# Kernel optimization log

Measured on AMD Instinct MI355X. Metric: run time of the kernel, lower is better.

The kernel has to match this reference:

```python
import jax, jax.numpy as jnp
import numpy as np

N, M, F_IN, F_OUT, B = 8192, 4096, 256, 128, 2048
NEG = -9e15
EPS = 1e-5


def leaky(x, slope=0.2):
    return jnp.where(x > 0, x, slope * x)


def batchnorm(x, gamma, beta):
    # BatchNorm1d training-mode semantics: biased batch stats over dim 0
    m = x.mean(axis=0)
    v = jnp.var(x, axis=0)
    return (x - m) * jax.lax.rsqrt(v + EPS) * gamma + beta


def setup_inputs() -> dict:
    key = jax.random.key(0)
    ks = jax.random.split(key, 12)
    inp = {}
    inp["Sinput"] = jax.random.normal(ks[0], (N, F_IN), dtype=jnp.float32)
    inp["Rinput"] = jax.random.normal(ks[1], (M, F_IN), dtype=jnp.float32)
    inp["inter_adj"] = jax.random.randint(ks[2], (N, M), 0, 2).astype(jnp.int32)
    inp["city_adj"] = jax.random.randint(ks[3], (N, N), 0, 2).astype(jnp.int32)
    inp["province_adj"] = jax.random.randint(ks[4], (N, N), 0, 2).astype(jnp.int32)
    inp["source_index"] = jax.random.randint(ks[5], (B,), 0, N).astype(jnp.int32)
    s_w = 1.414 * np.sqrt(6.0 / (F_IN + F_OUT))  # xavier_uniform gain=1.414
    s_a = 1.414 * np.sqrt(6.0 / (2 * F_OUT + 1))
    inp["W1"] = jax.random.uniform(ks[6], (F_IN, F_OUT), jnp.float32, -s_w, s_w)
    inp["W2"] = jax.random.uniform(ks[7], (F_IN, F_OUT), jnp.float32, -s_w, s_w)
    inp["a"] = jax.random.uniform(ks[8], (2 * F_OUT, 1), jnp.float32, -s_a, s_a)
    inp["a3"] = jax.random.uniform(ks[9], (2 * F_OUT, 1), jnp.float32, -s_a, s_a)
    inp["a4"] = jax.random.uniform(ks[10], (2 * F_OUT, 1), jnp.float32, -s_a, s_a)
    inp["bn1_gamma"] = jnp.ones((F_OUT,), jnp.float32)
    inp["bn1_beta"] = jnp.zeros((F_OUT,), jnp.float32)
    inp["bn2_gamma"] = jnp.ones((F_OUT,), jnp.float32)
    inp["bn2_beta"] = jnp.zeros((F_OUT,), jnp.float32)
    return inp


def reference(Sinput, Rinput, inter_adj, city_adj, province_adj, source_index,
              W1, W2, a, a3, a4, bn1_gamma, bn1_beta, bn2_gamma, bn2_beta):
    F = W1.shape[1]
    h1 = Rinput @ W1            # [M, F]
    h2 = Sinput @ W2            # [N, F]
    # Decomposed GAT score: cat([h1[m], h2[n]]) @ a == h1[m]@a[:F] + h2[n]@a[F:]
    e12 = leaky((h2 @ a[F:, 0])[:, None] + (h1 @ a[:F, 0])[None, :])  # [N, M]
    att_inter = jax.nn.softmax(jnp.where(inter_adj > 0, e12, NEG), axis=1)
    h2_ = h2[source_index]      # [B, F]
    # cat([h2_, h2_]) @ a3 -> h2_ @ (a3[:F] + a3[F:]), constant along N axis
    s3 = leaky(h2_ @ (a3[:F, 0] + a3[F:, 0]))  # [B]
    s4 = leaky(h2_ @ (a4[:F, 0] + a4[F:, 0]))  # [B]
    Nn = Sinput.shape[0]
    e3 = jnp.broadcast_to(s3[:, None], (s3.shape[0], Nn))
    e4 = jnp.broadcast_to(s4[:, None], (s4.shape[0], Nn))
    att3 = jax.nn.softmax(jnp.where(city_adj[source_index] > 0, e3, NEG), axis=1)
    att4 = jax.nn.softmax(jnp.where(province_adj[source_index] > 0, e4, NEG), axis=1)
    InterRC = att_inter @ h1                    # [N, F]
    IntraNC = att3.T @ h2_ + att4.T @ h2_       # [N, F]
    v_output = leaky(batchnorm(att_inter.T @ h2, bn1_gamma, bn1_beta))  # [M, F]
    u_output = leaky(batchnorm(InterRC + IntraNC, bn2_gamma, bn2_beta))  # [N, F]
    h_prime = u_output @ v_output.T             # [N, M]
    return jax.nn.elu(h_prime)
```

## Files before the change

### kernel.cpp

```cpp
#include <hip/hip_runtime.h>
#include <stdint.h>

#define N_ 8192
#define M_ 4096
#define FIN_ 256
#define F_ 128
#define B_ 2048

typedef __attribute__((ext_vector_type(8))) short vs8;
typedef __attribute__((ext_vector_type(8))) __bf16 vb8;
typedef __attribute__((ext_vector_type(4))) float vf4;

union ABu { vs8 s; vb8 b; };

__device__ __forceinline__ vf4 mfma16(const ABu& a, const ABu& b, vf4 c) {
    return __builtin_amdgcn_mfma_f32_16x16x32_bf16(a.b, b.b, c, 0, 0, 0);
}
__device__ __forceinline__ unsigned short f2b(float x) {
    union { float f; unsigned u; } v; v.f = x;
    unsigned r = v.u + 0x7fffu + ((v.u >> 16) & 1u);
    return (unsigned short)(r >> 16);
}
__device__ __forceinline__ float lrelu(float x) { return x > 0.f ? x : 0.2f * x; }

__device__ __forceinline__ void glds16(const unsigned short* g, void* l) {
    __builtin_amdgcn_global_load_lds((const __attribute__((address_space(1))) unsigned int*)g,
                                     (__attribute__((address_space(3))) unsigned int*)l, 16, 0, 0);
}

__global__ void k_prep(const float* __restrict__ W1, const float* __restrict__ W2,
                       unsigned short* __restrict__ W1T, unsigned short* __restrict__ W2T,
                       float4* __restrict__ Z, int nz4) {
    int id = blockIdx.x * 256 + threadIdx.x;
    if (id < 65536) {
        const float* W = (id < 32768) ? W1 : W2;
        unsigned short* WT = (id < 32768) ? W1T : W2T;
        int o = id & 32767;
        int f = o >> 8, k = o & 255;
        WT[o] = f2b(W[k * F_ + f]);
    } else {
        int z = id - 65536;
        if (z < nz4) Z[z] = make_float4(0.f, 0.f, 0.f, 0.f);
    }
}

__global__ __launch_bounds__(256) void k_hgemmF(const float* __restrict__ Rin, const float* __restrict__ Sin,
                                                const unsigned short* __restrict__ W1T,
                                                const unsigned short* __restrict__ W2T,
                                                const float* __restrict__ a,
                                                float* __restrict__ h2,
                                                unsigned short* __restrict__ h1P, unsigned short* __restrict__ h2P,
                                                float* __restrict__ s1, float* __restrict__ s2) {
    __shared__ unsigned short tb[16][136];
    __shared__ float sred[4][16];
    int t = threadIdx.x;
    int w = t >> 6, l = t & 63, lr = l & 15, lg = l >> 4;
    int gr = blockIdx.x * 16;
    const float* X; const unsigned short* WT; unsigned short* HP; float* sout; const float* av;
    int row0; bool isH2;
    if (gr < M_) { X = Rin; WT = W1T; HP = h1P; sout = s1; av = a;      row0 = gr;      isH2 = false; }
    else         { X = Sin; WT = W2T; HP = h2P; sout = s2; av = a + F_; row0 = gr - M_; isH2 = true;  }
    int fbase = w * 32;
    vf4 acc[2] = {};
    const float* xp = X + (size_t)(row0 + lr) * FIN_ + lg * 8;
#pragma unroll
    for (int kk = 0; kk < FIN_; kk += 32) {
        float4 xa = *(const float4*)(xp + kk);
        float4 xb = *(const float4*)(xp + kk + 4);
        ABu af;
        af.s[0] = (short)f2b(xa.x); af.s[1] = (short)f2b(xa.y);
        af.s[2] = (short)f2b(xa.z); af.s[3] = (short)f2b(xa.w);
        af.s[4] = (short)f2b(xb.x); af.s[5] = (short)f2b(xb.y);
        af.s[6] = (short)f2b(xb.z); af.s[7] = (short)f2b(xb.w);
#pragma unroll
        for (int q = 0; q < 2; ++q) {
            ABu bf; bf.s = *(const vs8*)(WT + (fbase + q * 16 + lr) * FIN_ + kk + lg * 8);
            acc[q] = mfma16(af, bf, acc[q]);
        }
    }
    if (isH2) {
#pragma unroll
        for (int q = 0; q < 2; ++q)
#pragma unroll
            for (int r = 0; r < 4; ++r)
                h2[(size_t)(row0 + lg * 4 + r) * F_ + fbase + q * 16 + lr] = acc[q][r];
    }
#pragma unroll
    for (int q = 0; q < 2; ++q)
#pragma unroll
        for (int r = 0; r < 4; ++r)
            tb[lg * 4 + r][fbase + q * 16 + lr] = f2b(acc[q][r]);
    float a0 = av[fbase + lr], a1 = av[fbase + 16 + lr];
    float tv[4];
#pragma unroll
    for (int r = 0; r < 4; ++r) tv[r] = acc[0][r] * a0 + acc[1][r] * a1;
#pragma unroll
    for (int off = 1; off < 16; off <<= 1)
#pragma unroll
        for (int r = 0; r < 4; ++r) tv[r] += __shfl_xor(tv[r], off, 64);
    if ((l & 15) == 0)
#pragma unroll
        for (int r = 0; r < 4; ++r) sred[w][lg * 4 + r] = tv[r];
    __syncthreads();
    {
        int f = t >> 1, half = t & 1;
        vs8 o;
#pragma unroll
        for (int j = 0; j < 8; ++j) o[j] = (short)tb[half * 8 + j][f];
        *(vs8*)(HP + ((size_t)(row0 >> 5) * 128 + f) * 32 + (row0 & 16) + half * 8) = o;
    }
    if (t < 16) {
        float s = sred[0][t] + sred[1][t] + sred[2][t] + sred[3][t];
        sout[row0 + t] = s;
    }
}

__global__ __launch_bounds__(256) void k_adjgather(const int* __restrict__ inter, const float* __restrict__ s1,
                                                   const float* __restrict__ s2, unsigned short* __restrict__ bm,
                                                   float* __restrict__ rowmax, float* __restrict__ rowinv,
                                                   const int* __restrict__ city, const int* __restrict__ prov,
                                                   const int* __restrict__ src,
                                                   uint32_t* __restrict__ BMtc, uint32_t* __restrict__ BMtp,
                                                   float* __restrict__ w3, float* __restrict__ w4,
                                                   const float* __restrict__ h2, unsigned short* __restrict__ h2wP) {
    __shared__ float wred[8];
    int t = threadIdx.x;
    int wv = t >> 6, ln = t & 63;
    if (blockIdx.x < N_) {
        int n = blockIdx.x;
        const int* rp = inter + (size_t)n * M_ + t * 16;
        float sv[16]; unsigned mask = 0;
#pragma unroll
        for (int c = 0; c < 4; ++c) {
            int4 v = *(const int4*)(rp + c * 4);
            if (v.x > 0) mask |= 1u << (c * 4 + 0);
            if (v.y > 0) mask |= 1u << (c * 4 + 1);
            if (v.z > 0) mask |= 1u << (c * 4 + 2);
            if (v.w > 0) mask |= 1u << (c * 4 + 3);
            float4 s = *(const float4*)(s1 + t * 16 + c * 4);
            sv[c * 4 + 0] = s.x; sv[c * 4 + 1] = s.y; sv[c * 4 + 2] = s.z; sv[c * 4 + 3] = s.w;
        }
        bm[(size_t)n * 256 + t] = (unsigned short)(mask & 0xffffu);
        float mx = -3.0e38f;
#pragma unroll
        for (int j = 0; j < 16; ++j) if (mask & (1u << j)) mx = fmaxf(mx, sv[j]);
        for (int off = 32; off > 0; off >>= 1) mx = fmaxf(mx, __shfl_down(mx, off, 64));
        if (ln == 0) wred[wv] = mx;
        __syncthreads();
        float s1mx = fmaxf(fmaxf(wred[0], wred[1]), fmaxf(wred[2], wred[3]));
        float s2n = s2[n];
        float rmx = lrelu(s2n + s1mx);
        float sum = 0.f;
#pragma unroll
        for (int j = 0; j < 16; ++j) if (mask & (1u << j)) sum += __expf(lrelu(s2n + sv[j]) - rmx);
        for (int off = 32; off > 0; off >>= 1) sum += __shfl_down(sum, off, 64);
        if (ln == 0) wred[4 + wv] = sum;
        __syncthreads();
        if (t == 0) {
            float tot = wred[4] + wred[5] + wred[6] + wred[7];
            bool any = s1mx > -2.9e38f;
            rowmax[n] = any ? rmx : 0.f;
            rowinv[n] = (any && tot > 0.f) ? 1.0f / tot : 0.f;
        }
    } else if (blockIdx.x < N_ + 2 * B_) {
        int bb = blockIdx.x - N_;
        int b = bb & (B_ - 1);
        bool isC = bb < B_;
        const int* adj = isC ? city : prov;
        uint32_t* BM = isC ? BMtc : BMtp;
        float* wout = isC ? w3 : w4;
        const int* rowp = adj + (size_t)src[b] * N_;
        int cnt = 0;
#pragma unroll 4
        for (int i = 0; i < N_ / 256; ++i) {
            int v = rowp[i * 256 + t];
            unsigned long long bal = __ballot(v > 0);
            cnt += (v > 0);
            if (ln == 0) {
                int widx = i * 8 + wv * 2;
                BM[(size_t)widx * B_ + b] = (uint32_t)bal;
                BM[(size_t)(widx + 1) * B_ + b] = (uint32_t)(bal >> 32);
            }
        }
        float fc = (float)cnt;
        for (int off = 32; off > 0; off >>= 1) fc += __shfl_down(fc, off, 64);
        if (ln == 0) wred[wv] = fc;
        __syncthreads();
        if (t == 0) {
            float tot = wred[0] + wred[1] + wred[2] + wred[3];
            wout[b] = tot > 0.f ? 1.0f / tot : 0.f;
        }
    } else {
        int bblk = blockIdx.x - (N_ + 2 * B_);
        int f = t & 127, halfb = t >> 7;
        vs8 o0, o1;
#pragma unroll
        for (int i = 0; i < 8; ++i) {
            int b0 = bblk * 32 + halfb * 16 + i;
            o0[i] = (short)f2b(h2[(size_t)src[b0] * F_ + f]);
            int b1 = b0 + 8;
            o1[i] = (short)f2b(h2[(size_t)src[b1] * F_ + f]);
        }
        unsigned short* dst = h2wP + ((size_t)bblk * 128 + f) * 32 + halfb * 16;
        *(vs8*)dst = o0;
        *(vs8*)(dst + 8) = o1;
    }
}

__global__ __launch_bounds__(256) void k_attmat2(const unsigned char* __restrict__ bm8,
                                                 const float* __restrict__ s1, const float* __restrict__ s2,
                                                 const float* __restrict__ rowmax, const float* __restrict__ rowinv,
                                                 unsigned short* __restrict__ attP,
                                                 unsigned short* __restrict__ attT) {
    __shared__ unsigned short tile[64][33];
    int bx = blockIdx.x;
    int mt = bx & 63, nt = bx >> 6;
    int nb = nt * 32, mb = mt * 64;
    int t = threadIdx.x;
    int mo = t & 7, nl = t >> 3;
    int n = nb + nl;
    int m = mb + mo * 8;
    unsigned bits = bm8[(size_t)n * 512 + (m >> 3)];
    float s2n = s2[n], rmx = rowmax[n], rin = rowinv[n];
    float4 sa = *(const float4*)(s1 + m);
    float4 sb = *(const float4*)(s1 + m + 4);
    float sv[8] = {sa.x, sa.y, sa.z, sa.w, sb.x, sb.y, sb.z, sb.w};
    vs8 o;
#pragma unroll
    for (int j = 0; j < 8; ++j) {
        float v = (bits & (1u << j)) ? __expf(lrelu(s2n + sv[j]) - rmx) * rin : 0.f;
        o[j] = (short)f2b(v);
        tile[mo * 8 + j][nl] = (unsigned short)o[j];
    }
    *(vs8*)(attP + ((size_t)(m >> 5) * N_ + n) * 32 + (m & 31)) = o;
    __syncthreads();
    int mr = t >> 2, sg = t & 3;
    vs8 ot;
#pragma unroll
    for (int j = 0; j < 8; ++j) ot[j] = (short)tile[mr][sg * 8 + j];
    *(vs8*)(attT + ((size_t)nt * M_ + mb + mr) * 32 + sg * 8) = ot;
}

__global__ __launch_bounds__(256) void k_gemmABC(const unsigned short* __restrict__ attP,
                                                 const unsigned short* __restrict__ attT,
                                                 const unsigned short* __restrict__ h1P,
                                                 const unsigned short* __restrict__ h2P,
                                                 const uint32_t* __restrict__ BMtc, const uint32_t* __restrict__ BMtp,
                                                 const float* __restrict__ w3, const float* __restrict__ w4,
                                                 const unsigned short* __restrict__ h2wP,
                                                 float* __restrict__ uP, float* __restrict__ vP) {
    __shared__ __align__(16) unsigned short smem[16384];
    int t = threadIdx.x;
    int w = t >> 6, l = t & 63;
    int lr = l & 15, lg = l >> 4;
    int bx = blockIdx.x;
    if (bx < 768) {
        bool isA = bx < 512;
        int i = isA ? bx : bx - 512;
        int x, y, ns, kbase, rowsK;
        const unsigned short* Asrc; const unsigned short* Bsrc; float* Out;
        if (isA) { x = i & 63; y = i >> 6; ns = 16; kbase = y * 16; rowsK = N_;
                   Asrc = attP; Bsrc = h1P; Out = uP + (size_t)y * N_ * F_; }
        else     { x = i & 31; y = i >> 5; ns = 32; kbase = y * 32; rowsK = M_;
                   Asrc = attT; Bsrc = h2P; Out = vP + (size_t)y * M_ * F_; }
        int rb0 = x * 128;
        int rq = (w >> 1) * 64;
        int cb = (w & 1) * 64;
        auto stage = [&](int kb, int buf) {
#pragma unroll
            for (int ii = 0; ii < 4; ++ii) {
                int c = w * 4 + ii;
                const unsigned short* g; int loff;
                if (c < 8) { g = Asrc + ((size_t)kb * rowsK + rb0) * 32 + c * 512 + l * 8;
                             loff = buf * 8192 + c * 512; }
                else       { g = Bsrc + (size_t)kb * 4096 + (c - 8) * 512 + l * 8;
                             loff = buf * 8192 + 4096 + (c - 8) * 512; }
                glds16(g, smem + loff);
            }
        };
        vf4 acc[4][4] = {};
        stage(kbase, 0);
        __syncthreads();
        int cur = 0;
        for (int step = 0; step < ns; ++step) {
            if (step + 1 < ns) stage(kbase + step + 1, cur ^ 1);
            const unsigned short* base = smem + cur * 8192;
            ABu a[4], b[4];
#pragma unroll
            for (int s = 0; s < 4; ++s) a[s].s = *(const vs8*)(base + (rq + s * 16 + lr) * 32 + lg * 8);
#pragma unroll
            for (int q = 0; q < 4; ++q) b[q].s = *(const vs8*)(base + 4096 + (cb + q * 16 + lr) * 32 + lg * 8);
#pragma unroll
            for (int s = 0; s < 4; ++s)
#pragma unroll
                for (int q = 0; q < 4; ++q) acc[s][q] = mfma16(a[s], b[q], acc[s][q]);
            __syncthreads();
            cur ^= 1;
        }
#pragma unroll
        for (int s = 0; s < 4; ++s)
#pragma unroll
            for (int q = 0; q < 4; ++q)
#pragma unroll
                for (int r = 0; r < 4; ++r)
                    Out[(size_t)(rb0 + rq + s * 16 + lg * 4 + r) * F_ + cb + q * 16 + lr] = acc[s][q][r];
    } else {
        int i = bx - 768;
        int xc = i & 127, yc = i >> 7;
        int nb0 = xc * 64 + (w & 1) * 32;
        int fb = (w >> 1) * 64;
        int wi = nb0 >> 5;
        const uint32_t* bc = BMtc + (size_t)wi * B_;
        const uint32_t* bp = BMtp + (size_t)wi * B_;
        vf4 acc[2][4] = {};
        int b0s = yc * (B_ / 4);
        for (int b0 = b0s; b0 < b0s + B_ / 4; b0 += 32) {
            int bb = b0 + lg * 8;
            uint4 c0 = *(const uint4*)(bc + bb);
            uint4 c1 = *(const uint4*)(bc + bb + 4);
            uint4 p0 = *(const uint4*)(bp + bb);
            uint4 p1 = *(const uint4*)(bp + bb + 4);
            float4 wa = *(const float4*)(w3 + bb);
            float4 wb = *(const float4*)(w3 + bb + 4);
            float4 wc = *(const float4*)(w4 + bb);
            float4 wd = *(const float4*)(w4 + bb + 4);
            const unsigned short* hb = h2wP + (size_t)(b0 >> 5) * 128 * 32;
            ABu bf0, bf1, bf2, bf3;
            bf0.s = *(const vs8*)(hb + (size_t)(fb + lr) * 32 + lg * 8);
            bf1.s = *(const vs8*)(hb + (size_t)(fb + 16 + lr) * 32 + lg * 8);
            bf2.s = *(const vs8*)(hb + (size_t)(fb + 32 + lr) * 32 + lg * 8);
            bf3.s = *(const vs8*)(hb + (size_t)(fb + 48 + lr) * 32 + lg * 8);
            uint32_t cw[8] = {c0.x, c0.y, c0.z, c0.w, c1.x, c1.y, c1.z, c1.w};
            uint32_t pw[8] = {p0.x, p0.y, p0.z, p0.w, p1.x, p1.y, p1.z, p1.w};
            float w3v[8] = {wa.x, wa.y, wa.z, wa.w, wb.x, wb.y, wb.z, wb.w};
            float w4v[8] = {wc.x, wc.y, wc.z, wc.w, wd.x, wd.y, wd.z, wd.w};
            ABu af0, af1;
#pragma unroll
            for (int j = 0; j < 8; ++j) {
                float v0 = (((cw[j] >> lr) & 1u) ? w3v[j] : 0.f) + (((pw[j] >> lr) & 1u) ? w4v[j] : 0.f);
                float v1 = (((cw[j] >> (16 + lr)) & 1u) ? w3v[j] : 0.f) + (((pw[j] >> (16 + lr)) & 1u) ? w4v[j] : 0.f);
                af0.s[j] = (short)f2b(v0);
                af1.s[j] = (short)f2b(v1);
            }
            acc[0][0] = mfma16(af0, bf0, acc[0][0]);
            acc[1][0] = mfma16(af1, bf0, acc[1][0]);
            acc[0][1] = mfma16(af0, bf1, acc[0][1]);
            acc[1][1] = mfma16(af1, bf1, acc[1][1]);
            acc[0][2] = mfma16(af0, bf2, acc[0][2]);
            acc[1][2] = mfma16(af1, bf2, acc[1][2]);
            acc[0][3] = mfma16(af0, bf3, acc[0][3]);
            acc[1][3] = mfma16(af1, bf3, acc[1][3]);
        }
        float* Out = uP + (size_t)(8 + yc) * N_ * F_;
#pragma unroll
        for (int s = 0; s < 2; ++s)
#pragma unroll
            for (int q = 0; q < 4; ++q)
#pragma unroll
                for (int r = 0; r < 4; ++r)
                    Out[(size_t)(nb0 + s * 16 + lg * 4 + r) * F_ + fb + q * 16 + lr] = acc[s][q][r];
    }
}

__global__ __launch_bounds__(256) void k_bnreduce(const float* __restrict__ vP, const float* __restrict__ uP,
                                                  float* __restrict__ v_in, float* __restrict__ u_in,
                                                  float* __restrict__ stats) {
    __shared__ float r1[256], r2[256];
    int bx = blockIdx.x;
    int f = threadIdx.x & 127;
    int half = threadIdx.x >> 7;
    float s = 0.f, s2v = 0.f;
    if (bx < 256) {
        size_t stride = (size_t)M_ * F_;
        for (int r = bx * 2 + half; r < M_; r += 512) {
            float v = 0.f;
#pragma unroll
            for (int y = 0; y < 8; ++y) v += vP[(size_t)y * stride + (size_t)r * F_ + f];
            v_in[(size_t)r * F_ + f] = v;
            s += v; s2v += v * v;
        }
        r1[threadIdx.x] = s; r2[threadIdx.x] = s2v;
        __syncthreads();
        if (half == 0) {
            atomicAdd(&stats[f], r1[f] + r1[f + 128]);
            atomicAdd(&stats[128 + f], r2[f] + r2[f + 128]);
        }
    } else {
        int b = bx - 256;
        size_t stride = (size_t)N_ * F_;
        for (int r = b * 2 + half; r < N_; r += 1024) {
            float v = 0.f;
#pragma unroll
            for (int y = 0; y < 12; ++y) v += uP[(size_t)y * stride + (size_t)r * F_ + f];
            u_in[(size_t)r * F_ + f] = v;
            s += v; s2v += v * v;
        }
        r1[threadIdx.x] = s; r2[threadIdx.x] = s2v;
        __syncthreads();
        if (half == 0) {
            atomicAdd(&stats[256 + f], r1[f] + r1[f + 128]);
            atomicAdd(&stats[384 + f], r2[f] + r2[f + 128]);
        }
    }
}

__global__ __launch_bounds__(256) void k_bnapplyF(const float* __restrict__ v_in, const float* __restrict__ u_in,
                                                  const float* __restrict__ stats,
                                                  const float* __restrict__ g1, const float* __restrict__ b1,
                                                  const float* __restrict__ g2, const float* __restrict__ b2,
                                                  unsigned short* __restrict__ v_outb, unsigned short* __restrict__ u_outb) {
    __shared__ float sc[256], sh[256];
    int t = threadIdx.x;
    {
        int which = t >> 7, f = t & 127;
        const float* sum = stats + which * 256;
        const float* sq = sum + 128;
        const float* g = which ? g2 : g1;
        const float* be = which ? b2 : b1;
        float R = which ? (float)N_ : (float)M_;
        float mean = sum[f] / R;
        float var = sq[f] / R - mean * mean;
        float s = g[f] * rsqrtf(var + 1e-5f);
        sc[t] = s; sh[t] = be[f] - mean * s;
    }
    __syncthreads();
    int id4 = blockIdx.x * 256 + t;
    int idx = id4 * 4;
    int which = idx >= M_ * F_;
    int rel = which ? idx - M_ * F_ : idx;
    const float* P = which ? u_in : v_in;
    unsigned short* Q = which ? u_outb : v_outb;
    int f0 = (rel & 127) + which * 128;
    float4 p = *(const float4*)(P + rel);
    ushort4 o;
    o.x = f2b(lrelu(p.x * sc[f0 + 0] + sh[f0 + 0]));
    o.y = f2b(lrelu(p.y * sc[f0 + 1] + sh[f0 + 1]));
    o.z = f2b(lrelu(p.z * sc[f0 + 2] + sh[f0 + 2]));
    o.w = f2b(lrelu(p.w * sc[f0 + 3] + sh[f0 + 3]));
    *(ushort4*)(Q + rel) = o;
}

__global__ __launch_bounds__(256) void k_gemmD(const unsigned short* __restrict__ U,
                                               const unsigned short* __restrict__ V,
                                               float* __restrict__ out) {
    int w = threadIdx.x >> 6, l = threadIdx.x & 63;
    int lr = l & 15, lg = l >> 4;
    int nb = blockIdx.x * 64 + w * 16;
    int mb = blockIdx.y * 64;
    vf4 acc[4] = {};
#pragma unroll
    for (int k0 = 0; k0 < F_; k0 += 32) {
        ABu af; af.s = *(const vs8*)(U + (size_t)(nb + lr) * F_ + k0 + lg * 8);
#pragma unroll
        for (int q = 0; q < 4; ++q) {
            ABu bf; bf.s = *(const vs8*)(V + (size_t)(mb + q * 16 + lr) * F_ + k0 + lg * 8);
            acc[q] = mfma16(af, bf, acc[q]);
        }
    }
#pragma unroll
    for (int q = 0; q < 4; ++q)
#pragma unroll
        for (int r = 0; r < 4; ++r) {
            int row = nb + lg * 4 + r;
            int col = mb + q * 16 + lr;
            float x = acc[q][r];
            out[(size_t)row * M_ + col] = x > 0.f ? x : __expf(x) - 1.f;
        }
}

extern "C" void kernel_launch(void* const* d_in, const int* in_sizes, int n_in,
                              void* d_out, int out_size, void* d_ws, size_t ws_size,
                              hipStream_t stream) {
    const float* Sinput = (const float*)d_in[0];
    const float* Rinput = (const float*)d_in[1];
    const int* inter_adj = (const int*)d_in[2];
    const int* city_adj = (const int*)d_in[3];
    const int* prov_adj = (const int*)d_in[4];
    const int* src = (const int*)d_in[5];
    const float* W1 = (const float*)d_in[6];
    const float* W2 = (const float*)d_in[7];
    const float* a = (const float*)d_in[8];
    const float* g1 = (const float*)d_in[11];
    const float* b1 = (const float*)d_in[12];
    const float* g2 = (const float*)d_in[13];
    const float* b2 = (const float*)d_in[14];
    float* out = (float*)d_out;

    char* ws = (char*)d_ws;
    size_t o = 0;
    auto take = [&](size_t bytes) { char* p = ws + o; o += (bytes + 255) & ~(size_t)255; return p; };
    float* stats = (float*)take(512 * 4);
    size_t zero_bytes = o;
    float* u_in = (float*)take((size_t)N_ * F_ * 4);
    float* v_in = (float*)take((size_t)M_ * F_ * 4);
    float* uP = (float*)take((size_t)12 * N_ * F_ * 4);
    float* vP = (float*)take((size_t)8 * M_ * F_ * 4);
    float* h2 = (float*)take((size_t)N_ * F_ * 4);
    unsigned short* h1P = (unsigned short*)take((size_t)(M_ / 32) * 128 * 32 * 2);
    unsigned short* h2P = (unsigned short*)take((size_t)(N_ / 32) * 128 * 32 * 2);
    unsigned short* W1T = (unsigned short*)take((size_t)F_ * FIN_ * 2);
    unsigned short* W2T = (unsigned short*)take((size_t)F_ * FIN_ * 2);
    float* s1 = (float*)take(M_ * 4);
    float* s2 = (float*)take(N_ * 4);
    float* rowmax = (float*)take(N_ * 4);
    float* rowinv = (float*)take(N_ * 4);
    float* w3 = (float*)take(B_ * 4);
    float* w4 = (float*)take(B_ * 4);
    unsigned short* h2wP = (unsigned short*)take((size_t)(B_ / 32) * 128 * 32 * 2);
    unsigned short* u_outb = (unsigned short*)take((size_t)N_ * F_ * 2);
    unsigned short* v_outb = (unsigned short*)take((size_t)M_ * F_ * 2);
    uint32_t* BMtc = (uint32_t*)take((size_t)256 * B_ * 4);
    uint32_t* BMtp = (uint32_t*)take((size_t)256 * B_ * 4);
    unsigned short* bm = (unsigned short*)take((size_t)N_ * 256 * 2);
    unsigned short* attP = (unsigned short*)take((size_t)N_ * M_ * 2);
    unsigned short* attT = (unsigned short*)take((size_t)N_ * M_ * 2);
    (void)ws_size; (void)in_sizes; (void)n_in; (void)out_size;

    int nz4 = (int)(zero_bytes / 16);
    int zblocks = (nz4 + 255) / 256;
    k_prep<<<256 + zblocks, 256, 0, stream>>>(W1, W2, W1T, W2T, (float4*)d_ws, nz4);
    k_hgemmF<<<(M_ + N_) / 16, 256, 0, stream>>>(Rinput, Sinput, W1T, W2T, a, h2, h1P, h2P, s1, s2);
    k_adjgather<<<N_ + 2 * B_ + B_ / 32, 256, 0, stream>>>(inter_adj, s1, s2, bm, rowmax, rowinv,
                                                           city_adj, prov_adj, src, BMtc, BMtp, w3, w4,
                                                           h2, h2wP);
    k_attmat2<<<16384, 256, 0, stream>>>((const unsigned char*)bm, s1, s2, rowmax, rowinv, attP, attT);
    k_gemmABC<<<1280, 256, 0, stream>>>(attP, attT, h1P, h2P, BMtc, BMtp, w3, w4, h2wP, uP, vP);
    k_bnreduce<<<768, 256, 0, stream>>>(vP, uP, v_in, u_in, stats);
    k_bnapplyF<<<(M_ + N_) * F_ / 4 / 256, 256, 0, stream>>>(v_in, u_in, stats, g1, b1, g2, b2, v_outb, u_outb);
    k_gemmD<<<dim3(N_ / 64, M_ / 64), 256, 0, stream>>>(u_outb, v_outb, out);
}
```

Measured before the change: 330.5 us.

## Halve split-K partials and fold partial summation into BN apply

The split-K factor of the attention GEMMs and the intra-neighbour GEMM is halved, so each block covers twice as much K and writes half as many fp32 partial slabs. The BN reduce kernel no longer writes summed u_in/v_in buffers and only computes statistics. The apply kernel re-reads and sums the partials itself. This cuts partial-buffer write/read traffic and the intermediate buffers, at the cost of fewer blocks (640) in the GEMM kernel, which lowers parallelism and lengthens each block's K loop.

After: 322.3 us (median of 2 runs). 2.5% less time.

```diff
diff --git a/kernel.cpp b/kernel.cpp
--- a/kernel.cpp
+++ b/kernel.cpp
@@ -254,14 +254,14 @@
     int w = t >> 6, l = t & 63;
     int lr = l & 15, lg = l >> 4;
     int bx = blockIdx.x;
-    if (bx < 768) {
-        bool isA = bx < 512;
-        int i = isA ? bx : bx - 512;
+    if (bx < 384) {
+        bool isA = bx < 256;
+        int i = isA ? bx : bx - 256;
         int x, y, ns, kbase, rowsK;
         const unsigned short* Asrc; const unsigned short* Bsrc; float* Out;
-        if (isA) { x = i & 63; y = i >> 6; ns = 16; kbase = y * 16; rowsK = N_;
+        if (isA) { x = i & 63; y = i >> 6; ns = 32; kbase = y * 32; rowsK = N_;
                    Asrc = attP; Bsrc = h1P; Out = uP + (size_t)y * N_ * F_; }
-        else     { x = i & 31; y = i >> 5; ns = 32; kbase = y * 32; rowsK = M_;
+        else     { x = i & 31; y = i >> 5; ns = 64; kbase = y * 64; rowsK = M_;
                    Asrc = attT; Bsrc = h2P; Out = vP + (size_t)y * M_ * F_; }
         int rb0 = x * 128;
         int rq = (w >> 1) * 64;
@@ -305,7 +305,7 @@
                 for (int r = 0; r < 4; ++r)
                     Out[(size_t)(rb0 + rq + s * 16 + lg * 4 + r) * F_ + cb + q * 16 + lr] = acc[s][q][r];
     } else {
-        int i = bx - 768;
+        int i = bx - 384;
         int xc = i & 127, yc = i >> 7;
         int nb0 = xc * 64 + (w & 1) * 32;
         int fb = (w >> 1) * 64;
@@ -313,8 +313,8 @@
         const uint32_t* bc = BMtc + (size_t)wi * B_;
         const uint32_t* bp = BMtp + (size_t)wi * B_;
         vf4 acc[2][4] = {};
-        int b0s = yc * (B_ / 4);
-        for (int b0 = b0s; b0 < b0s + B_ / 4; b0 += 32) {
+        int b0s = yc * (B_ / 2);
+        for (int b0 = b0s; b0 < b0s + B_ / 2; b0 += 32) {
             int bb = b0 + lg * 8;
             uint4 c0 = *(const uint4*)(bc + bb);
             uint4 c1 = *(const uint4*)(bc + bb + 4);
@@ -351,7 +351,7 @@
             acc[0][3] = mfma16(af0, bf3, acc[0][3]);
             acc[1][3] = mfma16(af1, bf3, acc[1][3]);
         }
-        float* Out = uP + (size_t)(8 + yc) * N_ * F_;
+        float* Out = uP + (size_t)(4 + yc) * N_ * F_;
 #pragma unroll
         for (int s = 0; s < 2; ++s)
 #pragma unroll
@@ -362,8 +362,7 @@
     }
 }
 
-__global__ __launch_bounds__(256) void k_bnreduce(const float* __restrict__ vP, const float* __restrict__ uP,
-                                                  float* __restrict__ v_in, float* __restrict__ u_in,
+__global__ __launch_bounds__(256) void k_bnstats3(const float* __restrict__ vP, const float* __restrict__ uP,
                                                   float* __restrict__ stats) {
     __shared__ float r1[256], r2[256];
     int bx = blockIdx.x;
@@ -375,8 +374,7 @@
         for (int r = bx * 2 + half; r < M_; r += 512) {
             float v = 0.f;
 #pragma unroll
-            for (int y = 0; y < 8; ++y) v += vP[(size_t)y * stride + (size_t)r * F_ + f];
-            v_in[(size_t)r * F_ + f] = v;
+            for (int y = 0; y < 4; ++y) v += vP[(size_t)y * stride + (size_t)r * F_ + f];
             s += v; s2v += v * v;
         }
         r1[threadIdx.x] = s; r2[threadIdx.x] = s2v;
@@ -388,11 +386,10 @@
     } else {
         int b = bx - 256;
         size_t stride = (size_t)N_ * F_;
-        for (int r = b * 2 + half; r < N_; r += 1024) {
+        for (int r = b * 2 + half; r < N_; r += 512) {
             float v = 0.f;
 #pragma unroll
-            for (int y = 0; y < 12; ++y) v += uP[(size_t)y * stride + (size_t)r * F_ + f];
-            u_in[(size_t)r * F_ + f] = v;
+            for (int y = 0; y < 6; ++y) v += uP[(size_t)y * stride + (size_t)r * F_ + f];
             s += v; s2v += v * v;
         }
         r1[threadIdx.x] = s; r2[threadIdx.x] = s2v;
@@ -404,7 +401,7 @@
     }
 }
 
-__global__ __launch_bounds__(256) void k_bnapplyF(const float* __restrict__ v_in, const float* __restrict__ u_in,
+__global__ __launch_bounds__(256) void k_bnapplyP(const float* __restrict__ vP, const float* __restrict__ uP,
                                                   const float* __restrict__ stats,
                                                   const float* __restrict__ g1, const float* __restrict__ b1,
                                                   const float* __restrict__ g2, const float* __restrict__ b2,
@@ -428,10 +425,26 @@
     int idx = id4 * 4;
     int which = idx >= M_ * F_;
     int rel = which ? idx - M_ * F_ : idx;
-    const float* P = which ? u_in : v_in;
-    unsigned short* Q = which ? u_outb : v_outb;
     int f0 = (rel & 127) + which * 128;
-    float4 p = *(const float4*)(P + rel);
+    float4 p = make_float4(0.f, 0.f, 0.f, 0.f);
+    unsigned short* Q;
+    if (!which) {
+        size_t stride = (size_t)M_ * F_;
+#pragma unroll
+        for (int y = 0; y < 4; ++y) {
+            float4 q = *(const float4*)(vP + (size_t)y * stride + rel);
+            p.x += q.x; p.y += q.y; p.z += q.z; p.w += q.w;
+        }
+        Q = v_outb;
+    } else {
+        size_t stride = (size_t)N_ * F_;
+#pragma unroll
+        for (int y = 0; y < 6; ++y) {
+            float4 q = *(const float4*)(uP + (size_t)y * stride + rel);
+            p.x += q.x; p.y += q.y; p.z += q.z; p.w += q.w;
+        }
+        Q = u_outb;
+    }
     ushort4 o;
     o.x = f2b(lrelu(p.x * sc[f0 + 0] + sh[f0 + 0]));
     o.y = f2b(lrelu(p.y * sc[f0 + 1] + sh[f0 + 1]));
@@ -491,10 +504,8 @@
     auto take = [&](size_t bytes) { char* p = ws + o; o += (bytes + 255) & ~(size_t)255; return p; };
     float* stats = (float*)take(512 * 4);
     size_t zero_bytes = o;
-    float* u_in = (float*)take((size_t)N_ * F_ * 4);
-    float* v_in = (float*)take((size_t)M_ * F_ * 4);
-    float* uP = (float*)take((size_t)12 * N_ * F_ * 4);
-    float* vP = (float*)take((size_t)8 * M_ * F_ * 4);
+    float* uP = (float*)take((size_t)6 * N_ * F_ * 4);
+    float* vP = (float*)take((size_t)4 * M_ * F_ * 4);
     float* h2 = (float*)take((size_t)N_ * F_ * 4);
     unsigned short* h1P = (unsigned short*)take((size_t)(M_ / 32) * 128 * 32 * 2);
     unsigned short* h2P = (unsigned short*)take((size_t)(N_ / 32) * 128 * 32 * 2);
@@ -524,8 +535,8 @@
                                                            city_adj, prov_adj, src, BMtc, BMtp, w3, w4,
                                                            h2, h2wP);
     k_attmat2<<<16384, 256, 0, stream>>>((const unsigned char*)bm, s1, s2, rowmax, rowinv, attP, attT);
-    k_gemmABC<<<1280, 256, 0, stream>>>(attP, attT, h1P, h2P, BMtc, BMtp, w3, w4, h2wP, uP, vP);
-    k_bnreduce<<<768, 256, 0, stream>>>(vP, uP, v_in, u_in, stats);
-    k_bnapplyF<<<(M_ + N_) * F_ / 4 / 256, 256, 0, stream>>>(v_in, u_in, stats, g1, b1, g2, b2, v_outb, u_outb);
+    k_gemmABC<<<640, 256, 0, stream>>>(attP, attT, h1P, h2P, BMtc, BMtp, w3, w4, h2wP, uP, vP);
+    k_bnstats3<<<512, 256, 0, stream>>>(vP, uP, stats);
+    k_bnapplyP<<<(M_ + N_) * F_ / 4 / 256, 256, 0, stream>>>(vP, uP, stats, g1, b1, g2, b2, v_outb, u_outb);
     k_gemmD<<<dim3(N_ / 64, M_ / 64), 256, 0, stream>>>(u_outb, v_outb, out);
 }
```
